# Optimization experiments

Hardware: AMD Instinct MI355X
Metric: run time of the kernel (lower is better)

Reference implementation:

```python
import jax, jax.numpy as jnp
import numpy as np

B, T, C = 8, 4096, 512


def setup_inputs() -> dict:
    key = jax.random.key(0)
    k1, k2, k3 = jax.random.split(key, 3)
    inputs = jax.random.normal(k1, (B, T, C), dtype=jnp.float32)
    # stable-ish recurrence: |A| < 1
    A_real = jax.random.uniform(k2, (C,), dtype=jnp.float32, minval=0.5, maxval=0.99)
    A_imag = jax.random.uniform(k3, (C,), dtype=jnp.float32, minval=-0.1, maxval=0.1)
    h0_real = jnp.zeros((B, C), dtype=jnp.float32)
    h0_imag = jnp.zeros((B, C), dtype=jnp.float32)
    return {"inputs": inputs, "A_real": A_real, "A_imag": A_imag,
            "h0_real": h0_real, "h0_imag": h0_imag}


def reference(inputs, A_real, A_imag, h0_real, h0_imag):
    # Diagonal complex linear recurrence:
    #   h[t] = A * h[t-1] + x[t]   (x real, added to real part only)
    # Output: states at every step, stacked (real, imag) -> (B, T, C, 2)
    def step(carry, x_t):
        hr, hi = carry
        nr = hr * A_real - hi * A_imag + x_t
        ni = A_imag * hr + A_real * hi
        return (nr, ni), (nr, ni)

    xs = jnp.swapaxes(inputs, 0, 1)  # (T, B, C)
    _, (real_seq, imag_seq) = jax.lax.scan(step, (h0_real, h0_imag), xs)
    real_seq = jnp.swapaxes(real_seq, 0, 1)  # (B, T, C)
    imag_seq = jnp.swapaxes(imag_seq, 0, 1)
    return jnp.stack([real_seq, imag_seq], axis=-1)  # (B, T, C, 2)
```

## Files before the change

kernel.cpp:

```cpp
#include <hip/hip_runtime.h>

#define BB 8
#define TT 4096
#define CC 512
#define NCHUNK 128
#define LCHUNK (TT / NCHUNK)

typedef float floatx4 __attribute__((ext_vector_type(4)));

__global__ __launch_bounds__(256, 4) void rec_ends(const float* __restrict__ x,
                                                   const float* __restrict__ Ar,
                                                   const float* __restrict__ Ai,
                                                   float4* __restrict__ s_end) {
    const int tid   = threadIdx.x;
    const int blk   = blockIdx.x;
    const int b     = blk / NCHUNK;
    const int chunk = blk % NCHUNK;
    const int t0    = chunk * LCHUNK;

    const float2 a_r = ((const float2*)Ar)[tid];
    const float2 a_i = ((const float2*)Ai)[tid];
    const float2* xp = (const float2*)(x + (size_t)(b * TT + t0) * CC) + tid;

    float hr0 = 0.f, hi0 = 0.f, hr1 = 0.f, hi1 = 0.f;
#pragma unroll 8
    for (int t = 0; t < LCHUNK; ++t) {
        float2 xv = xp[(size_t)t * (CC / 2)];
        float nr0 = fmaf(hr0, a_r.x, fmaf(-hi0, a_i.x, xv.x));
        float ni0 = fmaf(a_i.x, hr0, a_r.x * hi0);
        float nr1 = fmaf(hr1, a_r.y, fmaf(-hi1, a_i.y, xv.y));
        float ni1 = fmaf(a_i.y, hr1, a_r.y * hi1);
        hr0 = nr0; hi0 = ni0; hr1 = nr1; hi1 = ni1;
    }
    s_end[(size_t)(chunk * BB + b) * (CC / 2) + tid] = make_float4(hr0, hi0, hr1, hi1);
}

__global__ __launch_bounds__(256, 4) void rec_emit(const float* __restrict__ x,
                                                   const float* __restrict__ Ar,
                                                   const float* __restrict__ Ai,
                                                   const float* __restrict__ h0r,
                                                   const float* __restrict__ h0i,
                                                   const float4* __restrict__ s_end,
                                                   float4* __restrict__ out) {
    const int tid   = threadIdx.x;
    const int blk   = blockIdx.x;
    const int b     = blk / NCHUNK;
    const int chunk = blk % NCHUNK;
    const int t0    = chunk * LCHUNK;

    const float2 a_r = ((const float2*)Ar)[tid];
    const float2 a_i = ((const float2*)Ai)[tid];

    const float2* xp = (const float2*)(x + (size_t)(b * TT + t0) * CC) + tid;
    float2 xs[LCHUNK];
#pragma unroll
    for (int t = 0; t < LCHUNK; ++t)
        xs[t] = xp[(size_t)t * (CC / 2)];

    float p0r = a_r.x, p0i = a_i.x, p1r = a_r.y, p1i = a_i.y;
#pragma unroll
    for (int s = 0; s < 5; ++s) {
        float n0r = p0r * p0r - p0i * p0i, n0i = 2.f * p0r * p0i;
        float n1r = p1r * p1r - p1i * p1i, n1i = 2.f * p1r * p1i;
        p0r = n0r; p0i = n0i; p1r = n1r; p1i = n1i;
    }

    float2 h0rv = ((const float2*)(h0r + (size_t)b * CC))[tid];
    float2 h0iv = ((const float2*)(h0i + (size_t)b * CC))[tid];
    float hr0 = h0rv.x, hr1 = h0rv.y, hi0 = h0iv.x, hi1 = h0iv.y;

    const float4* sp = s_end + tid;
#pragma unroll 4
    for (int j = 0; j < chunk; ++j) {
        float4 s = sp[(size_t)(j * BB + b) * (CC / 2)];
        float nr0 = p0r * hr0 - p0i * hi0 + s.x;
        float ni0 = p0i * hr0 + p0r * hi0 + s.y;
        float nr1 = p1r * hr1 - p1i * hi1 + s.z;
        float ni1 = p1i * hr1 + p1r * hi1 + s.w;
        hr0 = nr0; hi0 = ni0; hr1 = nr1; hi1 = ni1;
    }

    floatx4* op = (floatx4*)(out + (size_t)(b * TT + t0) * (CC / 2) + tid);
#pragma unroll
    for (int t = 0; t < LCHUNK; ++t) {
        float2 xv = xs[t];
        float nr0 = fmaf(hr0, a_r.x, fmaf(-hi0, a_i.x, xv.x));
        float ni0 = fmaf(a_i.x, hr0, a_r.x * hi0);
        float nr1 = fmaf(hr1, a_r.y, fmaf(-hi1, a_i.y, xv.y));
        float ni1 = fmaf(a_i.y, hr1, a_r.y * hi1);
        hr0 = nr0; hi0 = ni0; hr1 = nr1; hi1 = ni1;
        floatx4 v = {nr0, ni0, nr1, ni1};
        __builtin_nontemporal_store(v, &op[(size_t)t * (CC / 2)]);
    }
}

extern "C" void kernel_launch(void* const* d_in, const int* in_sizes, int n_in,
                              void* d_out, int out_size, void* d_ws, size_t ws_size,
                              hipStream_t stream) {
    const float* x   = (const float*)d_in[0];
    const float* Ar  = (const float*)d_in[1];
    const float* Ai  = (const float*)d_in[2];
    const float* h0r = (const float*)d_in[3];
    const float* h0i = (const float*)d_in[4];
    float4* s_end = (float4*)d_ws;

    rec_ends<<<BB * NCHUNK, 256, 0, stream>>>(x, Ar, Ai, s_end);
    rec_emit<<<BB * NCHUNK, 256, 0, stream>>>(x, Ar, Ai, h0r, h0i, s_end,
                                              (float4*)d_out);
}
```

Baseline: 206.7 us.

## Replace per-block redundant chunk prefix with a dedicated sequential carry scan kernel

Before, each emit block recombined the end states of all preceding chunks, which is quadratic total work over the chunk carries. The change adds a third kernel that scans the 128 chunk-end states once per batch, in place in the output buffer, and writes each chunk's starting state. The emit kernel then reads a single start state instead of looping over its predecessors. In exchange, the carry propagation becomes a 128-step serial chain run by only 8 blocks, which adds latency and an extra launch.

```diff
diff --git a/kernel.cpp b/kernel.cpp
--- a/kernel.cpp
+++ b/kernel.cpp
@@ -5,17 +5,19 @@
 #define CC 512
 #define NCHUNK 128
 #define LCHUNK (TT / NCHUNK)
+#define NL (CC / 2)
 
 typedef float floatx4 __attribute__((ext_vector_type(4)));
 
-__global__ __launch_bounds__(256, 4) void rec_ends(const float* __restrict__ x,
-                                                   const float* __restrict__ Ar,
-                                                   const float* __restrict__ Ai,
-                                                   float4* __restrict__ s_end) {
+__global__ __launch_bounds__(256, 4) void rec_ends(
+    const float* __restrict__ x,
+    const float* __restrict__ Ar,
+    const float* __restrict__ Ai,
+    float4* __restrict__ out)
+{
     const int tid   = threadIdx.x;
-    const int blk   = blockIdx.x;
-    const int b     = blk / NCHUNK;
-    const int chunk = blk % NCHUNK;
+    const int b     = blockIdx.x / NCHUNK;
+    const int chunk = blockIdx.x % NCHUNK;
     const int t0    = chunk * LCHUNK;
 
     const float2 a_r = ((const float2*)Ar)[tid];
@@ -25,37 +27,28 @@
     float hr0 = 0.f, hi0 = 0.f, hr1 = 0.f, hi1 = 0.f;
 #pragma unroll 8
     for (int t = 0; t < LCHUNK; ++t) {
-        float2 xv = xp[(size_t)t * (CC / 2)];
+        float2 xv = xp[(size_t)t * NL];
         float nr0 = fmaf(hr0, a_r.x, fmaf(-hi0, a_i.x, xv.x));
         float ni0 = fmaf(a_i.x, hr0, a_r.x * hi0);
         float nr1 = fmaf(hr1, a_r.y, fmaf(-hi1, a_i.y, xv.y));
         float ni1 = fmaf(a_i.y, hr1, a_r.y * hi1);
         hr0 = nr0; hi0 = ni0; hr1 = nr1; hi1 = ni1;
     }
-    s_end[(size_t)(chunk * BB + b) * (CC / 2) + tid] = make_float4(hr0, hi0, hr1, hi1);
+    out[(size_t)(b * TT + t0) * NL + tid] = make_float4(hr0, hi0, hr1, hi1);
 }
 
-__global__ __launch_bounds__(256, 4) void rec_emit(const float* __restrict__ x,
-                                                   const float* __restrict__ Ar,
-                                                   const float* __restrict__ Ai,
-                                                   const float* __restrict__ h0r,
-                                                   const float* __restrict__ h0i,
-                                                   const float4* __restrict__ s_end,
-                                                   float4* __restrict__ out) {
-    const int tid   = threadIdx.x;
-    const int blk   = blockIdx.x;
-    const int b     = blk / NCHUNK;
-    const int chunk = blk % NCHUNK;
-    const int t0    = chunk * LCHUNK;
+__global__ __launch_bounds__(256, 1) void rec_scan(
+    const float* __restrict__ Ar,
+    const float* __restrict__ Ai,
+    const float* __restrict__ h0r,
+    const float* __restrict__ h0i,
+    float4* __restrict__ out)
+{
+    const int tid = threadIdx.x;
+    const int b   = blockIdx.x;
 
     const float2 a_r = ((const float2*)Ar)[tid];
     const float2 a_i = ((const float2*)Ai)[tid];
-
-    const float2* xp = (const float2*)(x + (size_t)(b * TT + t0) * CC) + tid;
-    float2 xs[LCHUNK];
-#pragma unroll
-    for (int t = 0; t < LCHUNK; ++t)
-        xs[t] = xp[(size_t)t * (CC / 2)];
 
     float p0r = a_r.x, p0i = a_i.x, p1r = a_r.y, p1i = a_i.y;
 #pragma unroll
@@ -65,22 +58,50 @@
         p0r = n0r; p0i = n0i; p1r = n1r; p1i = n1i;
     }
 
-    float2 h0rv = ((const float2*)(h0r + (size_t)b * CC))[tid];
-    float2 h0iv = ((const float2*)(h0i + (size_t)b * CC))[tid];
-    float hr0 = h0rv.x, hr1 = h0rv.y, hi0 = h0iv.x, hi1 = h0iv.y;
+    const float2 h0rv = ((const float2*)(h0r + (size_t)b * CC))[tid];
+    const float2 h0iv = ((const float2*)(h0i + (size_t)b * CC))[tid];
+    float sr0 = h0rv.x, sr1 = h0rv.y, si0 = h0iv.x, si1 = h0iv.y;
 
-    const float4* sp = s_end + tid;
-#pragma unroll 4
-    for (int j = 0; j < chunk; ++j) {
-        float4 s = sp[(size_t)(j * BB + b) * (CC / 2)];
-        float nr0 = p0r * hr0 - p0i * hi0 + s.x;
-        float ni0 = p0i * hr0 + p0r * hi0 + s.y;
-        float nr1 = p1r * hr1 - p1i * hi1 + s.z;
-        float ni1 = p1i * hr1 + p1r * hi1 + s.w;
-        hr0 = nr0; hi0 = ni0; hr1 = nr1; hi1 = ni1;
+    float4* q = out + (size_t)b * TT * NL + tid;
+#pragma unroll 8
+    for (int j = 0; j < NCHUNK; ++j) {
+        float4 e = *q;
+        *q = make_float4(sr0, si0, sr1, si1);
+        float nr0 = p0r * sr0 - p0i * si0 + e.x;
+        float ni0 = p0i * sr0 + p0r * si0 + e.y;
+        float nr1 = p1r * sr1 - p1i * si1 + e.z;
+        float ni1 = p1i * sr1 + p1r * si1 + e.w;
+        sr0 = nr0; si0 = ni0; sr1 = nr1; si1 = ni1;
+        q += (size_t)LCHUNK * NL;
     }
+}
 
-    floatx4* op = (floatx4*)(out + (size_t)(b * TT + t0) * (CC / 2) + tid);
+__global__ __launch_bounds__(256, 4) void rec_emit(
+    const float* __restrict__ x,
+    const float* __restrict__ Ar,
+    const float* __restrict__ Ai,
+    const float4* __restrict__ start,
+    float4* __restrict__ out)
+{
+    const int tid   = threadIdx.x;
+    const int b     = blockIdx.x / NCHUNK;
+    const int chunk = blockIdx.x % NCHUNK;
+    const int t0    = chunk * LCHUNK;
+
+    const size_t slot_idx = (size_t)(b * TT + t0) * NL + tid;
+    float4 s = start[slot_idx];
+
+    const float2* xp = (const float2*)(x + (size_t)(b * TT + t0) * CC) + tid;
+    float2 xs[LCHUNK];
+#pragma unroll
+    for (int t = 0; t < LCHUNK; ++t)
+        xs[t] = xp[(size_t)t * NL];
+
+    const float2 a_r = ((const float2*)Ar)[tid];
+    const float2 a_i = ((const float2*)Ai)[tid];
+
+    float hr0 = s.x, hi0 = s.y, hr1 = s.z, hi1 = s.w;
+    floatx4* op = (floatx4*)(out + slot_idx);
 #pragma unroll
     for (int t = 0; t < LCHUNK; ++t) {
         float2 xv = xs[t];
@@ -90,7 +111,7 @@
         float ni1 = fmaf(a_i.y, hr1, a_r.y * hi1);
         hr0 = nr0; hi0 = ni0; hr1 = nr1; hi1 = ni1;
         floatx4 v = {nr0, ni0, nr1, ni1};
-        __builtin_nontemporal_store(v, &op[(size_t)t * (CC / 2)]);
+        __builtin_nontemporal_store(v, &op[(size_t)t * NL]);
     }
 }
 
@@ -102,9 +123,9 @@
     const float* Ai  = (const float*)d_in[2];
     const float* h0r = (const float*)d_in[3];
     const float* h0i = (const float*)d_in[4];
-    float4* s_end = (float4*)d_ws;
+    float4* out = (float4*)d_out;
 
-    rec_ends<<<BB * NCHUNK, 256, 0, stream>>>(x, Ar, Ai, s_end);
-    rec_emit<<<BB * NCHUNK, 256, 0, stream>>>(x, Ar, Ai, h0r, h0i, s_end,
-                                              (float4*)d_out);
+    rec_ends<<<BB * NCHUNK, 256, 0, stream>>>(x, Ar, Ai, out);
+    rec_scan<<<BB, 256, 0, stream>>>(Ar, Ai, h0r, h0i, out);
+    rec_emit<<<BB * NCHUNK, 256, 0, stream>>>(x, Ar, Ai, out, out);
 }
```

After: 210.7 us. No clear change (+1.9%).
